# Kernel optimization log

Hardware: AMD Instinct MI355X
Metric: run time of the kernel (lower is better)

## Reference

```python
import jax, jax.numpy as jnp
import numpy as np

B, N_IN, N_OUT = 16, 7000, 28000
C_IN, C_OUT, S = 64, 64, 9
NNZ = 3 * N_OUT  # ~3 source verts per upsampled vert (barycentric)


def setup_inputs() -> dict:
    key = jax.random.key(0)
    k = jax.random.split(key, 6)
    x = jax.random.normal(k[0], (B, N_IN, C_IN), dtype=jnp.float32)
    values = jax.random.uniform(k[1], (NNZ,), dtype=jnp.float32)
    row = jax.random.randint(k[2], (NNZ,), 0, N_OUT)
    col = jax.random.randint(k[3], (NNZ,), 0, N_IN)
    spiral_indices = jax.random.randint(k[4], (N_OUT, S), 0, N_OUT)
    weight = jax.random.normal(k[5], (S * C_IN, C_OUT), dtype=jnp.float32) * 0.02
    bias = jnp.zeros((C_OUT,), dtype=jnp.float32)
    return {"x": x, "values": values, "weight": weight, "bias": bias,
            "row": row, "col": col, "spiral_indices": spiral_indices}


def reference(x, values, weight, bias, row, col, spiral_indices):
    # Pool: gather source verts, scale by sparse matrix values, scatter-add to output verts
    n_out = spiral_indices.shape[0]
    gathered = x[:, col, :] * values[None, :, None]            # [B, nnz, C]
    pooled = jnp.zeros((x.shape[0], n_out, x.shape[2]), x.dtype).at[:, row, :].add(gathered)  # [B, N_out, C]
    # SpiralConv: gather spiral neighborhood, flatten, linear
    feat = pooled[:, spiral_indices.reshape(-1), :]            # [B, N_out*S, C]
    feat = feat.reshape(x.shape[0], n_out, -1)                 # [B, N_out, S*C]
    out = jax.nn.elu(jnp.einsum('bnf,fo->bno', feat, weight) + bias)
    return out
```

## Files before the change

### kernel.cpp

```cpp
#include <hip/hip_runtime.h>
#include <math.h>

#define B      16
#define N_IN   7000
#define N_OUT  28000
#define C      64
#define S      9
#define NNZ    (3 * N_OUT)
#define F      (S * C)
#define KB     (F / 32)

#define MT     219

typedef short bf16x8 __attribute__((ext_vector_type(8)));
typedef float f32x4  __attribute__((ext_vector_type(4)));

static __device__ __forceinline__ unsigned short f2bf(float f) {
    unsigned u = __float_as_uint(f);
    u += 0x7fffu + ((u >> 16) & 1u);
    return (unsigned short)(u >> 16);
}

__global__ void hist_kernel(const int* __restrict__ row, int* __restrict__ cnt) {
    int i = blockIdx.x * 256 + threadIdx.x;
    if (i < NNZ) atomicAdd(&cnt[row[i]], 1);
}

__global__ void scan_kernel(const int* __restrict__ cnt,
                            int* __restrict__ offs, int* __restrict__ cursor) {
    __shared__ int tmp[1024];
    const int t = threadIdx.x;
    const int base = t * 28;
    const bool live = (t < 1000);

    int c[28];
    int partial = 0;
    if (live) {
        #pragma unroll
        for (int j = 0; j < 28; ++j) { c[j] = cnt[base + j]; partial += c[j]; }
    }
    tmp[t] = partial;
    __syncthreads();
    #pragma unroll
    for (int off = 1; off < 1024; off <<= 1) {
        int v = (t >= off) ? tmp[t - off] : 0;
        __syncthreads();
        tmp[t] += v;
        __syncthreads();
    }
    if (live) {
        int run = tmp[t] - partial;
        #pragma unroll
        for (int j = 0; j < 28; ++j) {
            offs[base + j]   = run;
            cursor[base + j] = run;
            run += c[j];
        }
        if (t == 999) offs[N_OUT] = run;
    }
}

__global__ void place_kernel(const int* __restrict__ row, const int* __restrict__ col,
                             const float* __restrict__ values,
                             int* __restrict__ cursor,
                             int* __restrict__ ecol, float* __restrict__ eval) {
    int i = blockIdx.x * 256 + threadIdx.x;
    if (i < NNZ) {
        int pos = atomicAdd(&cursor[row[i]], 1);
        ecol[pos] = col[i];
        eval[pos] = values[i];
    }
}

__global__ void pool_kernel(const float* __restrict__ x,
                            const int*   __restrict__ ecol,
                            const float* __restrict__ eval,
                            const int*   __restrict__ offs,
                            unsigned short* __restrict__ pooled) {
    const int bg     = blockIdx.x & 7;
    const int rowblk = blockIdx.x >> 3;
    const int wave = threadIdx.x >> 6;
    const int lane = threadIdx.x & 63;
    const int rsub = lane >> 5;
    const int bsub = (lane >> 4) & 1;
    const int sl   = lane & 15;

    const int r = rowblk * 8 + wave * 2 + rsub;
    const int b = bg + 8 * bsub;

    const int start = offs[r], end = offs[r + 1];

    float4 acc = make_float4(0.f, 0.f, 0.f, 0.f);
    const float* xb = x + (size_t)b * N_IN * C + sl * 4;

    for (int e = start; e < end; ++e) {
        const int   cl = ecol[e];
        const float v  = eval[e];
        const float4 xv = *(const float4*)(xb + (size_t)cl * C);
        acc.x = fmaf(xv.x, v, acc.x);
        acc.y = fmaf(xv.y, v, acc.y);
        acc.z = fmaf(xv.z, v, acc.z);
        acc.w = fmaf(xv.w, v, acc.w);
    }

    ushort4 o;
    o.x = f2bf(acc.x); o.y = f2bf(acc.y);
    o.z = f2bf(acc.z); o.w = f2bf(acc.w);
    *(ushort4*)(pooled + ((size_t)b * N_OUT + r) * C + sl * 4) = o;
}

__global__ void packw_kernel(const float* __restrict__ w, unsigned short* __restrict__ pw) {
    const int kb   = blockIdx.x;
    const int nt   = threadIdx.x >> 6;
    const int lane = threadIdx.x & 63;
    const int lm   = lane & 15;
    const int quad = lane >> 4;

    unsigned short v[8];
    #pragma unroll
    for (int j = 0; j < 8; ++j) {
        const int k = kb * 32 + quad * 8 + j;
        const int n = nt * 16 + lm;
        v[j] = f2bf(w[(size_t)k * C + n]);
    }
    unsigned short* dst = pw + ((size_t)(kb * 4 + nt) * 64 + lane) * 8;
    #pragma unroll
    for (int j = 0; j < 8; ++j) dst[j] = v[j];
}

__global__ __launch_bounds__(256, 4)
void spiral_mfma(const unsigned short* __restrict__ pooled,
                 const bf16x8*         __restrict__ packedW,
                 const int*            __restrict__ sp,
                 const float*          __restrict__ bias,
                 float*                __restrict__ out) {
    const int L = blockIdx.x;
    int b, mtile;
    if (L < 8 * MT) { b = L & 7;                  mtile = L >> 3; }
    else            { b = 8 + ((L - 8 * MT) & 7); mtile = (L - 8 * MT) >> 3; }

    const int wave = threadIdx.x >> 6;
    const int lane = threadIdx.x & 63;
    const int lm   = lane & 15;
    const int quad = lane >> 4;
    const int m_base = mtile * 128 + wave * 32;

    int spv[S];
    {
        int r = m_base + (lane & 31);
        if (r >= N_OUT) r = N_OUT - 1;
        #pragma unroll
        for (int s = 0; s < S; ++s) spv[s] = sp[r * S + s];
    }

    const unsigned short* poolb = pooled + (size_t)b * N_OUT * C;

    f32x4 acc[2][4];
    #pragma unroll
    for (int t = 0; t < 2; ++t)
        #pragma unroll
        for (int nt = 0; nt < 4; ++nt)
            acc[t][nt] = (f32x4){0.f, 0.f, 0.f, 0.f};

    int    rowi[2][2];
    bf16x8 abuf[2][2][2];

    #pragma unroll
    for (int t = 0; t < 2; ++t)
        rowi[0][t] = __shfl(spv[0], t * 16 + lm, 64);
    #pragma unroll
    for (int half = 0; half < 2; ++half) {
        const int c0 = half * 32 + quad * 8;
        #pragma unroll
        for (int t = 0; t < 2; ++t)
            abuf[0][half][t] = *(const bf16x8*)(poolb + (size_t)rowi[0][t] * C + c0);
    }

    #pragma unroll
    for (int s = 0; s < S; ++s) {
        const int cur = s & 1, nxt = cur ^ 1;

        bf16x8 bbuf[2][4];
        #pragma unroll
        for (int half = 0; half < 2; ++half)
            #pragma unroll
            for (int nt = 0; nt < 4; ++nt)
                bbuf[half][nt] = packedW[((s * 2 + half) * 4 + nt) * 64 + lane];

        if (s + 1 < S) {
            #pragma unroll
            for (int t = 0; t < 2; ++t)
                rowi[nxt][t] = __shfl(spv[s + 1], t * 16 + lm, 64);
            #pragma unroll
            for (int half = 0; half < 2; ++half) {
                const int c0 = half * 32 + quad * 8;
                #pragma unroll
                for (int t = 0; t < 2; ++t)
                    abuf[nxt][half][t] =
                        *(const bf16x8*)(poolb + (size_t)rowi[nxt][t] * C + c0);
            }
        }

        #pragma unroll
        for (int half = 0; half < 2; ++half)
            #pragma unroll
            for (int nt = 0; nt < 4; ++nt)
                #pragma unroll
                for (int t = 0; t < 2; ++t)
                    acc[t][nt] = __builtin_amdgcn_mfma_f32_16x16x32_bf16(
                        abuf[cur][half][t], bbuf[half][nt], acc[t][nt], 0, 0, 0);
    }

    #pragma unroll
    for (int nt = 0; nt < 4; ++nt) {
        const int n = nt * 16 + lm;
        const float bs = bias[n];
        #pragma unroll
        for (int t = 0; t < 2; ++t) {
            #pragma unroll
            for (int reg = 0; reg < 4; ++reg) {
                const int r = m_base + t * 16 + quad * 4 + reg;
                if (r < N_OUT) {
                    float v = acc[t][nt][reg] + bs;
                    v = v > 0.f ? v : (__expf(v) - 1.0f);
                    out[((size_t)b * N_OUT + r) * C + n] = v;
                }
            }
        }
    }
}

extern "C" void kernel_launch(void* const* d_in, const int* in_sizes, int n_in,
                              void* d_out, int out_size, void* d_ws, size_t ws_size,
                              hipStream_t stream) {
    const float* x      = (const float*)d_in[0];
    const float* values = (const float*)d_in[1];
    const float* weight = (const float*)d_in[2];
    const float* bias   = (const float*)d_in[3];
    const int*   row    = (const int*)d_in[4];
    const int*   col    = (const int*)d_in[5];
    const int*   sp     = (const int*)d_in[6];
    float*       out    = (float*)d_out;

    char* ws = (char*)d_ws;
    size_t off = 0;
    unsigned short* pooled  = (unsigned short*)(ws + off); off += (size_t)B * N_OUT * C * 2;
    unsigned short* packedW = (unsigned short*)(ws + off); off += (size_t)KB * 4 * 64 * 8 * 2;
    int*   offs   = (int*)(ws + off); off += ((size_t)(N_OUT + 1) * 4 + 124) / 128 * 128;
    int*   cursor = (int*)(ws + off); off += (size_t)N_OUT * 4 + 128;
    int*   cnt    = (int*)(ws + off); off += (size_t)N_OUT * 4 + 128;
    int*   ecol   = (int*)(ws + off); off += (size_t)NNZ * 4;
    float* eval   = (float*)(ws + off); off += (size_t)NNZ * 4;

    (void)hipMemsetAsync(cnt, 0, (size_t)N_OUT * 4, stream);
    hist_kernel <<<(NNZ + 255) / 256, 256, 0, stream>>>(row, cnt);
    scan_kernel <<<1, 1024, 0, stream>>>(cnt, offs, cursor);
    place_kernel<<<(NNZ + 255) / 256, 256, 0, stream>>>(row, col, values, cursor, ecol, eval);

    packw_kernel<<<KB, 256, 0, stream>>>(weight, packedW);

    pool_kernel<<<(N_OUT / 8) * 8, 256, 0, stream>>>(x, ecol, eval, offs, pooled);

    spiral_mfma<<<B * MT, 256, 0, stream>>>(pooled,
        reinterpret_cast<const bf16x8*>(packedW), sp, bias, out);
}
```

Baseline: 319.7 us.

## Stage packed weights in LDS, enlarge spiral tiles, unroll pooling gathers

```diff
diff --git a/kernel.cpp b/kernel.cpp
--- a/kernel.cpp
+++ b/kernel.cpp
@@ -10,7 +10,7 @@
 #define F      (S * C)
 #define KB     (F / 32)
 
-#define MT     219
+#define MT     110
 
 typedef short bf16x8 __attribute__((ext_vector_type(8)));
 typedef float f32x4  __attribute__((ext_vector_type(4)));
@@ -93,20 +93,35 @@
     float4 acc = make_float4(0.f, 0.f, 0.f, 0.f);
     const float* xb = x + (size_t)b * N_IN * C + sl * 4;
 
-    for (int e = start; e < end; ++e) {
-        const int   cl = ecol[e];
-        const float v  = eval[e];
-        const float4 xv = *(const float4*)(xb + (size_t)cl * C);
-        acc.x = fmaf(xv.x, v, acc.x);
-        acc.y = fmaf(xv.y, v, acc.y);
-        acc.z = fmaf(xv.z, v, acc.z);
-        acc.w = fmaf(xv.w, v, acc.w);
-    }
-
-    ushort4 o;
-    o.x = f2bf(acc.x); o.y = f2bf(acc.y);
-    o.z = f2bf(acc.z); o.w = f2bf(acc.w);
-    *(ushort4*)(pooled + ((size_t)b * N_OUT + r) * C + sl * 4) = o;
+    for (int e = start; e < end; e += 4) {
+        const int nn = end - e;
+        int   cl[4]; float vv[4];
+        #pragma unroll
+        for (int j = 0; j < 4; ++j) {
+            const int ee = (j < nn) ? e + j : e;
+            cl[j] = ecol[ee];
+            vv[j] = (j < nn) ? eval[ee] : 0.f;
+        }
+        float4 xv[4];
+        #pragma unroll
+        for (int j = 0; j < 4; ++j)
+            xv[j] = *(const float4*)(xb + (size_t)cl[j] * C);
+        #pragma unroll
+        for (int j = 0; j < 4; ++j) {
+            acc.x = fmaf(xv[j].x, vv[j], acc.x);
+            acc.y = fmaf(xv[j].y, vv[j], acc.y);
+            acc.z = fmaf(xv[j].z, vv[j], acc.z);
+            acc.w = fmaf(xv[j].w, vv[j], acc.w);
+        }
+    }
+
+    unsigned long long ov =
+        (unsigned long long)f2bf(acc.x)
+        | ((unsigned long long)f2bf(acc.y) << 16)
+        | ((unsigned long long)f2bf(acc.z) << 32)
+        | ((unsigned long long)f2bf(acc.w) << 48);
+    __builtin_nontemporal_store(ov,
+        (unsigned long long*)(pooled + ((size_t)b * N_OUT + r) * C + sl * 4));
 }
 
 __global__ void packw_kernel(const float* __restrict__ w, unsigned short* __restrict__ pw) {
@@ -128,7 +143,7 @@
     for (int j = 0; j < 8; ++j) dst[j] = v[j];
 }
 
-__global__ __launch_bounds__(256, 4)
+__global__ __launch_bounds__(512, 4)
 void spiral_mfma(const unsigned short* __restrict__ pooled,
                  const bf16x8*         __restrict__ packedW,
                  const int*            __restrict__ sp,
@@ -143,7 +158,15 @@
     const int lane = threadIdx.x & 63;
     const int lm   = lane & 15;
     const int quad = lane >> 4;
-    const int m_base = mtile * 128 + wave * 32;
+    const int m_base = mtile * 256 + wave * 32;
+
+    __shared__ bf16x8 bw[KB * 4 * 64];
+    {
+        const int t = threadIdx.x;
+        #pragma unroll
+        for (int i = 0; i < 9; ++i)
+            bw[i * 512 + t] = packedW[i * 512 + t];
+    }
 
     int spv[S];
     {
@@ -176,16 +199,11 @@
             abuf[0][half][t] = *(const bf16x8*)(poolb + (size_t)rowi[0][t] * C + c0);
     }
 
+    __syncthreads();
+
     #pragma unroll
     for (int s = 0; s < S; ++s) {
         const int cur = s & 1, nxt = cur ^ 1;
-
-        bf16x8 bbuf[2][4];
-        #pragma unroll
-        for (int half = 0; half < 2; ++half)
-            #pragma unroll
-            for (int nt = 0; nt < 4; ++nt)
-                bbuf[half][nt] = packedW[((s * 2 + half) * 4 + nt) * 64 + lane];
 
         if (s + 1 < S) {
             #pragma unroll
@@ -202,13 +220,18 @@
         }
 
         #pragma unroll
-        for (int half = 0; half < 2; ++half)
+        for (int half = 0; half < 2; ++half) {
+            bf16x8 bb[4];
+            #pragma unroll
+            for (int nt = 0; nt < 4; ++nt)
+                bb[nt] = bw[((s * 2 + half) * 4 + nt) * 64 + lane];
             #pragma unroll
             for (int nt = 0; nt < 4; ++nt)
                 #pragma unroll
                 for (int t = 0; t < 2; ++t)
                     acc[t][nt] = __builtin_amdgcn_mfma_f32_16x16x32_bf16(
-                        abuf[cur][half][t], bbuf[half][nt], acc[t][nt], 0, 0, 0);
+                        abuf[cur][half][t], bb[nt], acc[t][nt], 0, 0, 0);
+        }
     }
 
     #pragma unroll
@@ -223,7 +246,8 @@
                 if (r < N_OUT) {
                     float v = acc[t][nt][reg] + bs;
                     v = v > 0.f ? v : (__expf(v) - 1.0f);
-                    out[((size_t)b * N_OUT + r) * C + n] = v;
+                    __builtin_nontemporal_store(v,
+                        out + ((size_t)b * N_OUT + r) * C + n);
                 }
             }
         }
@@ -261,6 +285,6 @@
 
     pool_kernel<<<(N_OUT / 8) * 8, 256, 0, stream>>>(x, ecol, eval, offs, pooled);
 
-    spiral_mfma<<<B * MT, 256, 0, stream>>>(pooled,
+    spiral_mfma<<<B * MT, 512, 0, stream>>>(pooled,
         reinterpret_cast<const bf16x8*>(packedW), sp, bias, out);
 }
```

After: 303.8 us. 5.0% less time.
